# Performance work log

Hardware: AMD Instinct MI355X
Metric: run time of the kernel (lower is better)

Reference implementation:

```python
import jax, jax.numpy as jnp
import numpy as np

N_NODES = 20000


def _gcn_norm(edge_index, n):
    """Add self loops and compute symmetric normalization (PyG GCNConv default)."""
    loop = jnp.arange(n, dtype=edge_index.dtype)
    src = jnp.concatenate([edge_index[0], loop])  # [E+N]
    dst = jnp.concatenate([edge_index[1], loop])  # [E+N]
    deg = jax.ops.segment_sum(jnp.ones_like(dst, dtype=jnp.float32), dst, num_segments=n)
    inv_sqrt = deg ** -0.5  # deg >= 1 thanks to self loops
    norm = inv_sqrt[src] * inv_sqrt[dst]  # [E+N]
    return src, dst, norm


def _gcn_conv(x, W, b, src, dst, norm, n):
    xw = x @ W                                   # [N, out] dense transform
    msg = xw[src] * norm[:, None]                # gather + scale  [E+N, out]
    out = jax.ops.segment_sum(msg, dst, num_segments=n)  # scatter-add
    return out + b


def setup_inputs() -> dict:
    key = jax.random.key(0)
    ks = jax.random.split(key, 6)
    n, f = N_NODES, 256
    x = jax.random.normal(ks[0], (n, f), dtype=jnp.float32)
    edge_index = jax.random.randint(ks[1], (2, 320000), 0, n, dtype=jnp.int64)
    def lin(k, fi, fo):
        return jax.random.normal(k, (fi, fo), dtype=jnp.float32) * (1.0 / np.sqrt(fi))
    return {
        "x": x,
        "edge_index": edge_index,
        "W1": lin(ks[2], 256, 1024), "b1": jnp.zeros((1024,), jnp.float32),
        "W2": lin(ks[3], 1024, 512), "b2": jnp.zeros((512,), jnp.float32),
        "W3": lin(ks[4], 512, 128), "b3": jnp.zeros((128,), jnp.float32),
        "Wc": lin(ks[5], 128, 64), "bc": jnp.zeros((64,), jnp.float32),
    }


def reference(x, edge_index, W1, b1, W2, b2, W3, b3, Wc, bc):
    n = x.shape[0]
    src, dst, norm = _gcn_norm(edge_index, n)  # same graph for all layers
    h = jax.nn.relu(_gcn_conv(x, W1, b1, src, dst, norm, n))
    h = jax.nn.relu(_gcn_conv(h, W2, b2, src, dst, norm, n))
    h = jax.nn.relu(_gcn_conv(h, W3, b3, src, dst, norm, n))
    return h @ Wc + bc  # classifier logits [N, num_classes]
```

## Files before the change

kernel.cpp:

```cpp
#include <hip/hip_runtime.h>
#include <hip/hip_fp16.h>

typedef _Float16 half8 __attribute__((ext_vector_type(8)));
typedef _Float16 half4 __attribute__((ext_vector_type(4)));
typedef float floatx4 __attribute__((ext_vector_type(4)));


__device__ __forceinline__ void gload_lds16(const _Float16* g, _Float16* l) {
    __builtin_amdgcn_global_load_lds(
        (__attribute__((address_space(1))) void*)(g),
        (__attribute__((address_space(3))) void*)(l), 16, 0, 0);
}

__global__ void init_kernel(int* __restrict__ cnt, int* __restrict__ pos, int n) {
    int i = blockIdx.x * blockDim.x + threadIdx.x;
    if (i < n) { cnt[i] = 0; pos[i] = 0; }
}

__global__ void hist_kernel(const int* __restrict__ dst, int* __restrict__ cnt, int E) {
    int e = blockIdx.x * blockDim.x + threadIdx.x;
    if (e < E) atomicAdd(&cnt[dst[e]], 1);
}

__global__ void isd_kernel(const int* __restrict__ cnt, float* __restrict__ isd, int n) {
    int i = blockIdx.x * blockDim.x + threadIdx.x;
    if (i < n) isd[i] = rsqrtf((float)(cnt[i] + 1));
}

__global__ void scan_kernel(const int* __restrict__ cnt, int* __restrict__ row_ptr,
                            int n, int E) {
    __shared__ int part[1024];
    int t = threadIdx.x;
    int chunk = (n + 1023) >> 10;
    int beg = t * chunk, end = min(beg + chunk, n);
    int s = 0;
    for (int i = beg; i < end; ++i) s += cnt[i];
    part[t] = s;
    __syncthreads();
    for (int off = 1; off < 1024; off <<= 1) {
        int v = (t >= off) ? part[t - off] : 0;
        __syncthreads();
        part[t] += v;
        __syncthreads();
    }
    int run = part[t] - s;
    for (int i = beg; i < end; ++i) { row_ptr[i] = run; run += cnt[i]; }
    if (t == 0) row_ptr[n] = E;
}

__global__ void place_kernel(const int* __restrict__ src, const int* __restrict__ dst,
                             const float* __restrict__ isd, const int* __restrict__ row_ptr,
                             int* __restrict__ pos, int* __restrict__ s_src,
                             float* __restrict__ s_nrm, int E) {
    int e = blockIdx.x * blockDim.x + threadIdx.x;
    if (e < E) {
        int s = src[e], d = dst[e];
        int p = row_ptr[d] + atomicAdd(&pos[d], 1);
        s_src[p] = s;
        s_nrm[p] = isd[s] * isd[d];
    }
}

__global__ void f2h_kernel(const float4* __restrict__ in, half4* __restrict__ out, int n4) {
    int i = blockIdx.x * blockDim.x + threadIdx.x;
    if (i < n4) {
        float4 v = in[i];
        half4 o = { (_Float16)v.x, (_Float16)v.y, (_Float16)v.z, (_Float16)v.w };
        out[i] = o;
    }
}

__global__ void wtrans_kernel(const float* __restrict__ W, _Float16* __restrict__ Wt,
                              int fi, int fo, int fo_pad) {
    int idx = blockIdx.x * blockDim.x + threadIdx.x;
    if (idx >= fo_pad * fi) return;
    int o = idx / fi, i = idx - o * fi;
    Wt[idx] = (o < fo) ? (_Float16)W[(size_t)i * fo + o] : (_Float16)0.f;
}

template <int LPN, bool BIASRELU>
__global__ __launch_bounds__(256)
void aggv_kernel(const half8* __restrict__ xin, half8* __restrict__ xout,
                 const int* __restrict__ row_ptr, const int* __restrict__ s_src,
                 const float* __restrict__ s_nrm, const float* __restrict__ isd,
                 const float* __restrict__ bias, int n) {
    int t = blockIdx.x * blockDim.x + threadIdx.x;
    int i = t / LPN;
    int r = t % LPN;
    if (i >= n) return;
    float w = isd[i]; w *= w;
    half8 v = xin[(size_t)i * LPN + r];
    float a0[8], a1[8], a2[8], a3[8];
#pragma unroll
    for (int j = 0; j < 8; ++j) {
        a0[j] = (float)v[j] * w;
        a1[j] = 0.f; a2[j] = 0.f; a3[j] = 0.f;
    }
    int c = row_ptr[i], end = row_ptr[i + 1];
    for (; c + 8 <= end; c += 8) {
        int s0 = s_src[c],     s1 = s_src[c + 1], s2 = s_src[c + 2], s3 = s_src[c + 3];
        int s4 = s_src[c + 4], s5 = s_src[c + 5], s6 = s_src[c + 6], s7 = s_src[c + 7];
        float n0 = s_nrm[c],     n1 = s_nrm[c + 1], n2 = s_nrm[c + 2], n3 = s_nrm[c + 3];
        float n4 = s_nrm[c + 4], n5 = s_nrm[c + 5], n6 = s_nrm[c + 6], n7 = s_nrm[c + 7];
        half8 v0 = xin[(size_t)s0 * LPN + r];
        half8 v1 = xin[(size_t)s1 * LPN + r];
        half8 v2 = xin[(size_t)s2 * LPN + r];
        half8 v3 = xin[(size_t)s3 * LPN + r];
        half8 v4 = xin[(size_t)s4 * LPN + r];
        half8 v5 = xin[(size_t)s5 * LPN + r];
        half8 v6 = xin[(size_t)s6 * LPN + r];
        half8 v7 = xin[(size_t)s7 * LPN + r];
#pragma unroll
        for (int j = 0; j < 8; ++j) {
            a0[j] = fmaf((float)v0[j], n0, a0[j]);
            a1[j] = fmaf((float)v1[j], n1, a1[j]);
            a2[j] = fmaf((float)v2[j], n2, a2[j]);
            a3[j] = fmaf((float)v3[j], n3, a3[j]);
            a0[j] = fmaf((float)v4[j], n4, a0[j]);
            a1[j] = fmaf((float)v5[j], n5, a1[j]);
            a2[j] = fmaf((float)v6[j], n6, a2[j]);
            a3[j] = fmaf((float)v7[j], n7, a3[j]);
        }
    }
    for (; c + 2 <= end; c += 2) {
        int s0 = s_src[c], s1 = s_src[c + 1];
        float n0 = s_nrm[c], n1 = s_nrm[c + 1];
        half8 v0 = xin[(size_t)s0 * LPN + r];
        half8 v1 = xin[(size_t)s1 * LPN + r];
#pragma unroll
        for (int j = 0; j < 8; ++j) {
            a0[j] = fmaf((float)v0[j], n0, a0[j]);
            a1[j] = fmaf((float)v1[j], n1, a1[j]);
        }
    }
    if (c < end) {
        int s0 = s_src[c];
        float n0 = s_nrm[c];
        half8 v0 = xin[(size_t)s0 * LPN + r];
#pragma unroll
        for (int j = 0; j < 8; ++j) a0[j] = fmaf((float)v0[j], n0, a0[j]);
    }
    half8 o;
#pragma unroll
    for (int j = 0; j < 8; ++j) {
        float s = (a0[j] + a1[j]) + (a2[j] + a3[j]);
        if (BIASRELU) s = fmaxf(s + bias[r * 8 + j], 0.f);
        o[j] = (_Float16)s;
    }
    xout[(size_t)i * LPN + r] = o;
}

template <bool BIAS, bool RELU, bool OUT_HALF>
__global__ __launch_bounds__(256, 4)
void hgemm_kernel(const _Float16* __restrict__ A, const _Float16* __restrict__ Bt,
                  const float* __restrict__ bias, void* __restrict__ C,
                  int M, int K, int Ncout, int ldc, int gy) {
    __shared__ _Float16 As[128 * 64];
    __shared__ _Float16 Bs[64 * 64];

    int nwg = gridDim.x;
    int orig = blockIdx.x;
    int q = nwg >> 3, r = nwg & 7;
    int xcd = orig & 7, seq = orig >> 3;
    int wgid = (xcd < r ? xcd * (q + 1) : r * (q + 1) + (xcd - r) * q) + seq;
    int bx = wgid / gy, by = wgid % gy;

    const int tid = threadIdx.x;
    const int wave = tid >> 6, lane = tid & 63;
    const int l15 = lane & 15, lk = lane >> 4;
    const int wr = wave >> 1, wc = wave & 1;
    const int bm = bx * 128, bn = by * 64;

    const int sk_swz = (((tid & 7) ^ ((tid >> 3) & 7)) << 3);
    const _Float16* aSrc = A + (size_t)(bm + (tid >> 3)) * K + sk_swz;
    const _Float16* bSrc = Bt + (size_t)(bn + (tid >> 3)) * K + sk_swz;

    const int rowA = wr * 64 + l15;
    const int rowB = wc * 32 + l15;
    const int xorK = (l15 & 7) << 3;

    floatx4 acc[4][2] = {};

    const int nt = K >> 6;
    for (int t = 0; t < nt; ++t) {
        int k0 = t << 6;
#pragma unroll
        for (int i = 0; i < 4; ++i)
            gload_lds16(aSrc + k0 + (size_t)i * 32 * K, As + (i * 256 + tid) * 8);
#pragma unroll
        for (int i = 0; i < 2; ++i)
            gload_lds16(bSrc + k0 + (size_t)i * 32 * K, Bs + (i * 256 + tid) * 8);
        __syncthreads();
#pragma unroll
        for (int ks = 0; ks < 2; ++ks) {
            const int kidx = ((lk << 3) + (ks << 5)) ^ xorK;
            half8 af[4], bf[2];
#pragma unroll
            for (int mi = 0; mi < 4; ++mi)
                af[mi] = *(const half8*)(&As[(rowA + mi * 16) * 64 + kidx]);
#pragma unroll
            for (int ni = 0; ni < 2; ++ni)
                bf[ni] = *(const half8*)(&Bs[(rowB + ni * 16) * 64 + kidx]);
#pragma unroll
            for (int mi = 0; mi < 4; ++mi)
#pragma unroll
                for (int ni = 0; ni < 2; ++ni)
                    acc[mi][ni] = __builtin_amdgcn_mfma_f32_16x16x32_f16(
                        af[mi], bf[ni], acc[mi][ni], 0, 0, 0);
        }
        __syncthreads();
    }

#pragma unroll
    for (int mi = 0; mi < 4; ++mi) {
#pragma unroll
        for (int ni = 0; ni < 2; ++ni) {
            int col = bn + wc * 32 + ni * 16 + l15;
            int row0 = bm + wr * 64 + mi * 16 + lk * 4;
            floatx4 vv = acc[mi][ni];
            if (BIAS) {
                float bb = (col < Ncout) ? bias[col] : 0.f;
                vv[0] += bb; vv[1] += bb; vv[2] += bb; vv[3] += bb;
            }
            if (RELU) {
                vv[0] = fmaxf(vv[0], 0.f); vv[1] = fmaxf(vv[1], 0.f);
                vv[2] = fmaxf(vv[2], 0.f); vv[3] = fmaxf(vv[3], 0.f);
            }
            if (col < Ncout) {
#pragma unroll
                for (int rr = 0; rr < 4; ++rr) {
                    int row = row0 + rr;
                    if (row < M) {
                        if (OUT_HALF)
                            ((__half*)C)[(size_t)row * ldc + col] = __float2half(vv[rr]);
                        else
                            ((float*)C)[(size_t)row * ldc + col] = vv[rr];
                    }
                }
            }
        }
    }
}

extern "C" void kernel_launch(void* const* d_in, const int* in_sizes, int n_in,
                              void* d_out, int out_size, void* d_ws, size_t ws_size,
                              hipStream_t stream) {
    const float* x  = (const float*)d_in[0];
    const int*   ei = (const int*)d_in[1];
    const float* W1 = (const float*)d_in[2];
    const float* b1 = (const float*)d_in[3];
    const float* W2 = (const float*)d_in[4];
    const float* b2 = (const float*)d_in[5];
    const float* W3 = (const float*)d_in[6];
    const float* b3 = (const float*)d_in[7];
    const float* Wc = (const float*)d_in[8];
    const float* bc = (const float*)d_in[9];
    float* out = (float*)d_out;

    const int n = in_sizes[0] / 256;
    const int E = in_sizes[1] / 2;
    const int* src = ei;
    const int* dst = ei + E;
    const int Mpad = ((n + 127) / 128) * 128;
    const int gx = Mpad / 128;

    size_t off = 0;
    auto take = [&](size_t bytes) -> void* {
        void* p = (char*)d_ws + off;
        off += (bytes + 255) & ~(size_t)255;
        return p;
    };
    float* isd     = (float*)take((size_t)n * 4);
    int*   cnt     = (int*)take((size_t)n * 4);
    int*   pos     = (int*)take((size_t)n * 4);
    int*   row_ptr = (int*)take((size_t)(n + 1) * 4);
    int*   s_src   = (int*)take((size_t)E * 4);
    float* s_nrm   = (float*)take((size_t)E * 4);
    _Float16* xh   = (_Float16*)take((size_t)n * 256 * 2);
    _Float16* a1h  = (_Float16*)take((size_t)Mpad * 256 * 2);
    _Float16* h1h  = (_Float16*)take((size_t)Mpad * 1024 * 2);
    _Float16* g2h  = (_Float16*)take((size_t)Mpad * 512 * 2);
    _Float16* a2h  = (_Float16*)take((size_t)Mpad * 512 * 2);
    _Float16* g3h  = (_Float16*)take((size_t)Mpad * 128 * 2);
    _Float16* a3h  = (_Float16*)take((size_t)Mpad * 128 * 2);
    _Float16* w1t  = (_Float16*)take((size_t)1024 * 256 * 2);
    _Float16* w2t  = (_Float16*)take((size_t)512 * 1024 * 2);
    _Float16* w3t  = (_Float16*)take((size_t)128 * 512 * 2);
    _Float16* wct  = (_Float16*)take((size_t)64 * 128 * 2);

    init_kernel<<<(n + 255) / 256, 256, 0, stream>>>(cnt, pos, n);
    hist_kernel<<<(E + 255) / 256, 256, 0, stream>>>(dst, cnt, E);
    isd_kernel<<<(n + 255) / 256, 256, 0, stream>>>(cnt, isd, n);
    scan_kernel<<<1, 1024, 0, stream>>>(cnt, row_ptr, n, E);
    place_kernel<<<(E + 255) / 256, 256, 0, stream>>>(src, dst, isd, row_ptr, pos,
                                                      s_src, s_nrm, E);

    int n4 = n * 256 / 4;
    f2h_kernel<<<(n4 + 255) / 256, 256, 0, stream>>>((const float4*)x, (half4*)xh, n4);
    wtrans_kernel<<<(1024 * 256 + 255) / 256, 256, 0, stream>>>(W1, w1t, 256, 1024, 1024);
    wtrans_kernel<<<(512 * 1024 + 255) / 256, 256, 0, stream>>>(W2, w2t, 1024, 512, 512);
    wtrans_kernel<<<(128 * 512 + 255) / 256, 256, 0, stream>>>(W3, w3t, 512, 128, 128);
    wtrans_kernel<<<(64 * 128 + 255) / 256, 256, 0, stream>>>(Wc, wct, 128, 64, 64);

    aggv_kernel<32, false><<<(n * 32 + 255) / 256, 256, 0, stream>>>(
        (const half8*)xh, (half8*)a1h, row_ptr, s_src, s_nrm, isd, nullptr, n);
    hgemm_kernel<true, true, true><<<gx * 16, 256, 0, stream>>>(
        a1h, w1t, b1, h1h, n, 256, 1024, 1024, 16);

    hgemm_kernel<false, false, true><<<gx * 8, 256, 0, stream>>>(
        h1h, w2t, nullptr, g2h, n, 1024, 512, 512, 8);
    aggv_kernel<64, true><<<(n * 64 + 255) / 256, 256, 0, stream>>>(
        (const half8*)g2h, (half8*)a2h, row_ptr, s_src, s_nrm, isd, b2, n);

    hgemm_kernel<false, false, true><<<gx * 2, 256, 0, stream>>>(
        a2h, w3t, nullptr, g3h, n, 512, 128, 128, 2);
    aggv_kernel<16, true><<<(n * 16 + 255) / 256, 256, 0, stream>>>(
        (const half8*)g3h, (half8*)a3h, row_ptr, s_src, s_nrm, isd, b3, n);

    hgemm_kernel<true, false, false><<<gx * 1, 256, 0, stream>>>(
        a3h, wct, bc, out, n, 128, 64, 64, 1);
}
```

Baseline: 242.2 us.

## Split aggregation into column chunks and parallelize the CSR row-pointer scan

Replaces the single-block serial scan with a three-kernel block-sum, block-scan and row-pointer scan. Adds an aggregation kernel that splits the feature columns into eight chunks handled by separate blocks, so each pass gathers a narrower slice of every neighbor row and the working set of the gathered matrix is more likely to stay in cache. Edge-list loads use nontemporal hints. The unroll depth of the remaining aggregation kernel drops from 8 to 4. The cost is that the edge list is re-read once per chunk and there are more kernel launches.

Result: slower. 272.3 us (+12.4%).

```diff
diff --git a/kernel.cpp b/kernel.cpp
--- a/kernel.cpp
+++ b/kernel.cpp
@@ -27,25 +27,49 @@
     if (i < n) isd[i] = rsqrtf((float)(cnt[i] + 1));
 }
 
-__global__ void scan_kernel(const int* __restrict__ cnt, int* __restrict__ row_ptr,
-                            int n, int E) {
-    __shared__ int part[1024];
+__global__ void bsum_kernel(const int* __restrict__ cnt, int* __restrict__ bsum, int n) {
+    int i = blockIdx.x * 256 + threadIdx.x;
+    int v = (i < n) ? cnt[i] : 0;
+#pragma unroll
+    for (int o = 32; o > 0; o >>= 1) v += __shfl_down(v, o);
+    __shared__ int ws[4];
+    int lane = threadIdx.x & 63, w = threadIdx.x >> 6;
+    if (lane == 0) ws[w] = v;
+    __syncthreads();
+    if (threadIdx.x == 0) bsum[blockIdx.x] = ws[0] + ws[1] + ws[2] + ws[3];
+}
+
+__global__ void bscan_kernel(int* __restrict__ bsum, int nb) {
+    __shared__ int sh[256];
     int t = threadIdx.x;
-    int chunk = (n + 1023) >> 10;
-    int beg = t * chunk, end = min(beg + chunk, n);
-    int s = 0;
-    for (int i = beg; i < end; ++i) s += cnt[i];
-    part[t] = s;
+    int v = (t < nb) ? bsum[t] : 0;
+    sh[t] = v;
     __syncthreads();
-    for (int off = 1; off < 1024; off <<= 1) {
-        int v = (t >= off) ? part[t - off] : 0;
-        __syncthreads();
-        part[t] += v;
-        __syncthreads();
-    }
-    int run = part[t] - s;
-    for (int i = beg; i < end; ++i) { row_ptr[i] = run; run += cnt[i]; }
-    if (t == 0) row_ptr[n] = E;
+    for (int o = 1; o < 256; o <<= 1) {
+        int u = (t >= o) ? sh[t - o] : 0;
+        __syncthreads();
+        sh[t] += u;
+        __syncthreads();
+    }
+    if (t < nb) bsum[t] = sh[t] - v;
+}
+
+__global__ void rowptr_kernel(const int* __restrict__ cnt, const int* __restrict__ bsum,
+                              int* __restrict__ row_ptr, int n, int E) {
+    __shared__ int sh[256];
+    int t = threadIdx.x;
+    int i = blockIdx.x * 256 + t;
+    int v = (i < n) ? cnt[i] : 0;
+    sh[t] = v;
+    __syncthreads();
+    for (int o = 1; o < 256; o <<= 1) {
+        int u = (t >= o) ? sh[t - o] : 0;
+        __syncthreads();
+        sh[t] += u;
+        __syncthreads();
+    }
+    if (i < n) row_ptr[i] = bsum[blockIdx.x] + sh[t] - v;
+    if (blockIdx.x == 0 && t == 0) row_ptr[n] = E;
 }
 
 __global__ void place_kernel(const int* __restrict__ src, const int* __restrict__ dst,
@@ -76,6 +100,67 @@
     if (idx >= fo_pad * fi) return;
     int o = idx / fi, i = idx - o * fi;
     Wt[idx] = (o < fo) ? (_Float16)W[(size_t)i * fo + o] : (_Float16)0.f;
+}
+
+template <int LPN, bool BIASRELU>
+__global__ __launch_bounds__(256)
+void aggc_kernel(const half8* __restrict__ xin, half8* __restrict__ xout,
+                 const int* __restrict__ row_ptr, const int* __restrict__ s_src,
+                 const float* __restrict__ s_nrm, const float* __restrict__ isd,
+                 const float* __restrict__ bias, int n) {
+    const int D8 = 8 * LPN;
+    int ch = blockIdx.x & 7;
+    int nb = blockIdx.x >> 3;
+    int t = nb * 256 + threadIdx.x;
+    int i = t / LPN;
+    int r = t % LPN;
+    if (i >= n) return;
+    const int col8 = ch * LPN + r;
+    float w = isd[i]; w *= w;
+    half8 v = xin[(size_t)i * D8 + col8];
+    float a0[8], a1[8], a2[8], a3[8];
+#pragma unroll
+    for (int j = 0; j < 8; ++j) {
+        a0[j] = (float)v[j] * w;
+        a1[j] = 0.f; a2[j] = 0.f; a3[j] = 0.f;
+    }
+    int c = row_ptr[i], end = row_ptr[i + 1];
+    for (; c + 4 <= end; c += 4) {
+        int s0 = __builtin_nontemporal_load(&s_src[c]);
+        int s1 = __builtin_nontemporal_load(&s_src[c + 1]);
+        int s2 = __builtin_nontemporal_load(&s_src[c + 2]);
+        int s3 = __builtin_nontemporal_load(&s_src[c + 3]);
+        float n0 = __builtin_nontemporal_load(&s_nrm[c]);
+        float n1 = __builtin_nontemporal_load(&s_nrm[c + 1]);
+        float n2 = __builtin_nontemporal_load(&s_nrm[c + 2]);
+        float n3 = __builtin_nontemporal_load(&s_nrm[c + 3]);
+        half8 v0 = xin[(size_t)s0 * D8 + col8];
+        half8 v1 = xin[(size_t)s1 * D8 + col8];
+        half8 v2 = xin[(size_t)s2 * D8 + col8];
+        half8 v3 = xin[(size_t)s3 * D8 + col8];
+#pragma unroll
+        for (int j = 0; j < 8; ++j) {
+            a0[j] = fmaf((float)v0[j], n0, a0[j]);
+            a1[j] = fmaf((float)v1[j], n1, a1[j]);
+            a2[j] = fmaf((float)v2[j], n2, a2[j]);
+            a3[j] = fmaf((float)v3[j], n3, a3[j]);
+        }
+    }
+    for (; c < end; ++c) {
+        int s0 = __builtin_nontemporal_load(&s_src[c]);
+        float n0 = __builtin_nontemporal_load(&s_nrm[c]);
+        half8 v0 = xin[(size_t)s0 * D8 + col8];
+#pragma unroll
+        for (int j = 0; j < 8; ++j) a0[j] = fmaf((float)v0[j], n0, a0[j]);
+    }
+    half8 o;
+#pragma unroll
+    for (int j = 0; j < 8; ++j) {
+        float s = (a0[j] + a1[j]) + (a2[j] + a3[j]);
+        if (BIASRELU) s = fmaxf(s + bias[col8 * 8 + j], 0.f);
+        o[j] = (_Float16)s;
+    }
+    xout[(size_t)i * D8 + col8] = o;
 }
 
 template <int LPN, bool BIASRELU>
@@ -97,43 +182,22 @@
         a1[j] = 0.f; a2[j] = 0.f; a3[j] = 0.f;
     }
     int c = row_ptr[i], end = row_ptr[i + 1];
-    for (; c + 8 <= end; c += 8) {
-        int s0 = s_src[c],     s1 = s_src[c + 1], s2 = s_src[c + 2], s3 = s_src[c + 3];
-        int s4 = s_src[c + 4], s5 = s_src[c + 5], s6 = s_src[c + 6], s7 = s_src[c + 7];
-        float n0 = s_nrm[c],     n1 = s_nrm[c + 1], n2 = s_nrm[c + 2], n3 = s_nrm[c + 3];
-        float n4 = s_nrm[c + 4], n5 = s_nrm[c + 5], n6 = s_nrm[c + 6], n7 = s_nrm[c + 7];
+    for (; c + 4 <= end; c += 4) {
+        int s0 = s_src[c], s1 = s_src[c + 1], s2 = s_src[c + 2], s3 = s_src[c + 3];
+        float n0 = s_nrm[c], n1 = s_nrm[c + 1], n2 = s_nrm[c + 2], n3 = s_nrm[c + 3];
         half8 v0 = xin[(size_t)s0 * LPN + r];
         half8 v1 = xin[(size_t)s1 * LPN + r];
         half8 v2 = xin[(size_t)s2 * LPN + r];
         half8 v3 = xin[(size_t)s3 * LPN + r];
-        half8 v4 = xin[(size_t)s4 * LPN + r];
-        half8 v5 = xin[(size_t)s5 * LPN + r];
-        half8 v6 = xin[(size_t)s6 * LPN + r];
-        half8 v7 = xin[(size_t)s7 * LPN + r];
 #pragma unroll
         for (int j = 0; j < 8; ++j) {
             a0[j] = fmaf((float)v0[j], n0, a0[j]);
             a1[j] = fmaf((float)v1[j], n1, a1[j]);
             a2[j] = fmaf((float)v2[j], n2, a2[j]);
             a3[j] = fmaf((float)v3[j], n3, a3[j]);
-            a0[j] = fmaf((float)v4[j], n4, a0[j]);
-            a1[j] = fmaf((float)v5[j], n5, a1[j]);
-            a2[j] = fmaf((float)v6[j], n6, a2[j]);
-            a3[j] = fmaf((float)v7[j], n7, a3[j]);
         }
     }
-    for (; c + 2 <= end; c += 2) {
-        int s0 = s_src[c], s1 = s_src[c + 1];
-        float n0 = s_nrm[c], n1 = s_nrm[c + 1];
-        half8 v0 = xin[(size_t)s0 * LPN + r];
-        half8 v1 = xin[(size_t)s1 * LPN + r];
-#pragma unroll
-        for (int j = 0; j < 8; ++j) {
-            a0[j] = fmaf((float)v0[j], n0, a0[j]);
-            a1[j] = fmaf((float)v1[j], n1, a1[j]);
-        }
-    }
-    if (c < end) {
+    for (; c < end; ++c) {
         int s0 = s_src[c];
         float n0 = s_nrm[c];
         half8 v0 = xin[(size_t)s0 * LPN + r];
@@ -263,6 +327,7 @@
     const int* dst = ei + E;
     const int Mpad = ((n + 127) / 128) * 128;
     const int gx = Mpad / 128;
+    const int nb = (n + 255) / 256;
 
     size_t off = 0;
     auto take = [&](size_t bytes) -> void* {
@@ -274,6 +339,7 @@
     int*   cnt     = (int*)take((size_t)n * 4);
     int*   pos     = (int*)take((size_t)n * 4);
     int*   row_ptr = (int*)take((size_t)(n + 1) * 4);
+    int*   bsum    = (int*)take((size_t)256 * 4);
     int*   s_src   = (int*)take((size_t)E * 4);
     float* s_nrm   = (float*)take((size_t)E * 4);
     _Float16* xh   = (_Float16*)take((size_t)n * 256 * 2);
@@ -291,7 +357,9 @@
     init_kernel<<<(n + 255) / 256, 256, 0, stream>>>(cnt, pos, n);
     hist_kernel<<<(E + 255) / 256, 256, 0, stream>>>(dst, cnt, E);
     isd_kernel<<<(n + 255) / 256, 256, 0, stream>>>(cnt, isd, n);
-    scan_kernel<<<1, 1024, 0, stream>>>(cnt, row_ptr, n, E);
+    bsum_kernel<<<nb, 256, 0, stream>>>(cnt, bsum, n);
+    bscan_kernel<<<1, 256, 0, stream>>>(bsum, nb);
+    rowptr_kernel<<<nb, 256, 0, stream>>>(cnt, bsum, row_ptr, n, E);
     place_kernel<<<(E + 255) / 256, 256, 0, stream>>>(src, dst, isd, row_ptr, pos,
                                                       s_src, s_nrm, E);
 
@@ -302,15 +370,21 @@
     wtrans_kernel<<<(128 * 512 + 255) / 256, 256, 0, stream>>>(W3, w3t, 512, 128, 128);
     wtrans_kernel<<<(64 * 128 + 255) / 256, 256, 0, stream>>>(Wc, wct, 128, 64, 64);
 
-    aggv_kernel<32, false><<<(n * 32 + 255) / 256, 256, 0, stream>>>(
-        (const half8*)xh, (half8*)a1h, row_ptr, s_src, s_nrm, isd, nullptr, n);
+    {
+        int nblk = (n * 4 + 255) / 256;
+        aggc_kernel<4, false><<<nblk * 8, 256, 0, stream>>>(
+            (const half8*)xh, (half8*)a1h, row_ptr, s_src, s_nrm, isd, nullptr, n);
+    }
     hgemm_kernel<true, true, true><<<gx * 16, 256, 0, stream>>>(
         a1h, w1t, b1, h1h, n, 256, 1024, 1024, 16);
 
     hgemm_kernel<false, false, true><<<gx * 8, 256, 0, stream>>>(
         h1h, w2t, nullptr, g2h, n, 1024, 512, 512, 8);
-    aggv_kernel<64, true><<<(n * 64 + 255) / 256, 256, 0, stream>>>(
-        (const half8*)g2h, (half8*)a2h, row_ptr, s_src, s_nrm, isd, b2, n);
+    {
+        int nblk = (n * 8 + 255) / 256;
+        aggc_kernel<8, true><<<nblk * 8, 256, 0, stream>>>(
+            (const half8*)g2h, (half8*)a2h, row_ptr, s_src, s_nrm, isd, b2, n);
+    }
 
     hgemm_kernel<false, false, true><<<gx * 2, 256, 0, stream>>>(
         a2h, w3t, nullptr, g3h, n, 512, 128, 128, 2);
```
